# Kernel optimization log

Measured on AMD Instinct MI355X. Metric: run time of the kernel, lower is better.

## Reference

```python
import jax, jax.numpy as jnp
import numpy as np

K = 16          # neighbors (init kwarg k)
LEAK = 0.2      # LeakyReLU slope
EPS = 1e-5      # GroupNorm eps
GROUPS = 4


def knn_idx(coor_k, coor_q, k):
    # coor_* : (B, 3, N); returns (B, Nq, k) indices of k nearest keys per query
    qk = jnp.einsum('bdq,bdk->bqk', coor_q, coor_k)
    q2 = jnp.sum(coor_q * coor_q, axis=1)[:, :, None]
    k2 = jnp.sum(coor_k * coor_k, axis=1)[:, None, :]
    d2 = q2 + k2 - 2.0 * qk                     # (B, Nq, Nk) squared distances
    _, idx = jax.lax.top_k(-d2, k)
    return idx


def gather_feats(x_k, idx):
    # x_k (B, D, Nk), idx (B, Nq, k) -> (B, D, Nq, k)
    feat = jax.vmap(lambda fk, i: fk[i])(jnp.transpose(x_k, (0, 2, 1)), idx)  # (B,Nq,k,D)
    return jnp.transpose(feat, (0, 3, 1, 2))


def graph_feature(coor_q, x_q, coor_k, x_k, k):
    idx = knn_idx(coor_k, coor_q, k)
    feat = gather_feats(x_k, idx)                # (B, D, Nq, k)
    xq = x_q[:, :, :, None]
    return jnp.concatenate([feat - xq, jnp.broadcast_to(xq, feat.shape)], axis=1)


def group_norm(x, gamma, beta):
    B, C, N, Kk = x.shape
    xg = x.reshape(B, GROUPS, C // GROUPS, N, Kk)
    mu = xg.mean(axis=(2, 3, 4), keepdims=True)
    var = xg.var(axis=(2, 3, 4), keepdims=True)
    xn = ((xg - mu) * jax.lax.rsqrt(var + EPS)).reshape(B, C, N, Kk)
    return xn * gamma[None, :, None, None] + beta[None, :, None, None]


def conv_gn_lrelu(x, w, gamma, beta):
    y = jnp.einsum('oc,bcnk->bonk', w, x)        # 1x1 conv, no bias
    y = group_norm(y, gamma, beta)
    return jnp.where(y > 0, y, LEAK * y)


def fps(xyz, npoint):
    # xyz (B, N, 3) -> (B, npoint) farthest-point-sampling indices, start at 0
    B, N, _ = xyz.shape
    d0 = jnp.full((B, N), 1e10, dtype=xyz.dtype)

    def step(carry, _):
        dist, far = carry
        centroid = jnp.take_along_axis(xyz, far[:, None, None], axis=1)  # (B,1,3)
        d = jnp.sum((xyz - centroid) ** 2, axis=-1)
        dist = jnp.minimum(dist, d)
        nxt = jnp.argmax(dist, axis=-1).astype(jnp.int32)
        return (dist, nxt), far

    far0 = jnp.zeros((B,), dtype=jnp.int32)
    _, idxs = jax.lax.scan(step, (d0, far0), None, length=npoint)
    return jnp.transpose(idxs)                   # (B, npoint)


def fps_downsample(coor, x, num_group):
    # coor (B,3,N), x (B,D,N)
    fidx = fps(jnp.transpose(coor, (0, 2, 1)), num_group)   # (B, num_group)
    comb = jnp.concatenate([coor, x], axis=1)                # (B, 3+D, N)
    new = jax.vmap(lambda c, i: c[:, i])(comb, fidx)         # (B, 3+D, num_group)
    return new[:, :3], new[:, 3:]


def setup_inputs() -> dict:
    key = jax.random.key(0)
    ks = jax.random.split(key, 8)
    B, N = 16, 2048
    return {
        'x': jax.random.normal(ks[0], (B, N, 3), jnp.float32),
        'num0': 512,
        'num1': 128,
        'w_in': jax.random.normal(ks[1], (8, 3), jnp.float32) * 0.3,
        'b_in': jax.random.normal(ks[2], (8,), jnp.float32) * 0.1,
        'w1': jax.random.normal(ks[3], (32, 16), jnp.float32) * 0.2,
        'g1': jnp.ones((32,), jnp.float32), 'be1': jnp.zeros((32,), jnp.float32),
        'w2': jax.random.normal(ks[4], (64, 64), jnp.float32) * 0.12,
        'g2': jnp.ones((64,), jnp.float32), 'be2': jnp.zeros((64,), jnp.float32),
        'w3': jax.random.normal(ks[5], (64, 128), jnp.float32) * 0.09,
        'g3': jnp.ones((64,), jnp.float32), 'be3': jnp.zeros((64,), jnp.float32),
        'w4': jax.random.normal(ks[6], (128, 128), jnp.float32) * 0.09,
        'g4': jnp.ones((128,), jnp.float32), 'be4': jnp.zeros((128,), jnp.float32),
    }


def reference(x, num0, num1, w_in, b_in, w1, g1, be1, w2, g2, be2,
              w3, g3, be3, w4, g4, be4):
    coor = jnp.transpose(x, (0, 2, 1))                       # (B,3,N)
    f = jnp.einsum('oc,bcn->bon', w_in, coor) + b_in[None, :, None]  # (B,8,N)

    f = graph_feature(coor, f, coor, f, K)                   # (B,16,N,K)
    f = conv_gn_lrelu(f, w1, g1, be1).max(axis=-1)           # (B,32,N)

    coor_q, f_q = fps_downsample(coor, f, num0)
    f = graph_feature(coor_q, f_q, coor, f, K)               # (B,64,num0,K)
    f = conv_gn_lrelu(f, w2, g2, be2).max(axis=-1)           # (B,64,num0)
    coor = coor_q

    f = graph_feature(coor, f, coor, f, K)                   # (B,128,num0,K)
    f = conv_gn_lrelu(f, w3, g3, be3).max(axis=-1)           # (B,64,num0)

    coor_q, f_q = fps_downsample(coor, f, num1)
    f = graph_feature(coor_q, f_q, coor, f, K)               # (B,128,num1,K)
    f = conv_gn_lrelu(f, w4, g4, be4).max(axis=-1)           # (B,128,num1)

    return jnp.transpose(coor_q, (0, 2, 1)), jnp.transpose(f, (0, 2, 1))
```

## Files before the change

### kernel.cpp

```cpp
#include <hip/hip_runtime.h>

#define KNN 16
static constexpr int BB = 16;
static constexpr float LEAK = 0.2f;
static constexpr float EPSV = 1e-5f;
typedef unsigned long long u64;

__device__ __forceinline__ void ce_asc(u64 &a, u64 &b) {
  u64 x = a, y = b; bool sw = y < x; a = sw ? y : x; b = sw ? x : y;
}
__device__ __forceinline__ void ce_desc(u64 &a, u64 &b) {
  u64 x = a, y = b; bool sw = x < y; a = sw ? y : x; b = sw ? x : y;
}
__device__ __forceinline__ void bitonic_sort16(u64 *T) {
#pragma unroll
  for (int k = 2; k <= 16; k <<= 1) {
#pragma unroll
    for (int j = k >> 1; j > 0; j >>= 1) {
#pragma unroll
      for (int i = 0; i < 16; ++i) {
        int l = i ^ j;
        if (l > i) {
          if ((i & k) == 0) ce_asc(T[i], T[l]); else ce_desc(T[i], T[l]);
        }
      }
    }
  }
}
__device__ __forceinline__ void merge_sorted16(u64 *R, const u64 *T) {
#pragma unroll
  for (int i = 0; i < 16; ++i) {
    u64 t = T[15 - i];
    R[i] = t < R[i] ? t : R[i];
  }
#pragma unroll
  for (int j = 8; j > 0; j >>= 1) {
#pragma unroll
    for (int i = 0; i < 16; ++i) {
      int l = i ^ j;
      if (l > i) ce_asc(R[i], R[l]);
    }
  }
}
template<int KC>
__device__ __forceinline__ void merge_row(const u64* __restrict__ p, u64* R) {
#pragma unroll
  for (int s = 0; s < 16; ++s) R[s] = p[s];
#pragma unroll
  for (int c = 1; c < KC; ++c) {
    u64 T[16];
#pragma unroll
    for (int s = 0; s < 16; ++s) T[s] = p[(size_t)c*KNN + s];
    merge_sorted16(R, T);
  }
}

__device__ __forceinline__ void f0_dev(const float* __restrict__ x,
    const float* __restrict__ w_in, const float* __restrict__ b_in,
    float* __restrict__ f0, int bid) {
  int i = bid * 256 + threadIdx.x;
  float px = x[i*3+0], py = x[i*3+1], pz = x[i*3+2];
#pragma unroll
  for (int o = 0; o < 8; ++o) {
    f0[i*8+o] = w_in[o*3+0]*px + w_in[o*3+1]*py + w_in[o*3+2]*pz + b_in[o];
  }
}

__device__ void knn_part_dev(const float* __restrict__ qxyz, int Nq,
    const float* __restrict__ kxyz, int Nk, int KC, u64* __restrict__ part,
    char* sm, int bid) {
  float4* keys = (float4*)sm;
  int nqb = (Nq + 255) >> 8;
  int c  = bid % KC;
  int qb = (bid / KC) % nqb;
  int b  = bid / (KC * nqb);
  int nkc = Nk / KC;
  int kbase = c * nkc;
  for (int j = threadIdx.x; j < nkc; j += 256) {
    const float* kp = kxyz + (size_t)(b*Nk + kbase + j)*3;
    float kx = kp[0], ky = kp[1], kz = kp[2];
    keys[j] = make_float4(kx, ky, kz, kx*kx + ky*ky + kz*kz);
  }
  __syncthreads();
  int q = (qb << 8) + threadIdx.x;
  if (q >= Nq) return;
  const float* qp = qxyz + (size_t)(b*Nq + q)*3;
  float qx = qp[0], qy = qp[1], qz = qp[2];
  float q2 = qx*qx + qy*qy + qz*qz;
  u64 R[16];
#pragma unroll
  for (int s = 0; s < 16; ++s) R[s] = 0xFFFFFFFFFFFFFFFFull;
  for (int j0 = 0; j0 < nkc; j0 += 16) {
    u64 T[16];
#pragma unroll
    for (int u = 0; u < 16; ++u) {
      float4 kk = keys[j0 + u];
      float qk = qx*kk.x + qy*kk.y + qz*kk.z;
      float d2 = q2 + kk.w - 2.0f*qk;
      int bb = __float_as_int(d2);
      unsigned k32 = (unsigned)bb ^ (unsigned)((bb >> 31) | 0x80000000);
      T[u] = ((u64)k32 << 32) | (unsigned)(kbase + j0 + u);
    }
    bitonic_sort16(T);
    merge_sorted16(R, T);
  }
  u64* op = part + ((size_t)(b*Nq + q)*KC + c)*KNN;
#pragma unroll
  for (int s = 0; s < KNN; ++s) op[s] = R[s];
}

__device__ __forceinline__ u64 fps_max64(u64 a, u64 b) { return a > b ? a : b; }
template<int CTRL>
__device__ __forceinline__ float fps_dpp_fmax(float v) {
  int nb = __builtin_amdgcn_update_dpp(0, __float_as_int(v), CTRL, 0xF, 0xF, false);
  return fmaxf(v, __int_as_float(nb));
}
template<int P, bool SAVE>
__device__ void fps_seg_dev(const float* __restrict__ xyz, int np,
    int t0, int t1, int* __restrict__ fidx,
    float* __restrict__ g_dl, int* __restrict__ g_far,
    int* __restrict__ inv, float* __restrict__ cq, char* sm, int b) {
  constexpr int NN = P * 256;
  float4* sc  = (float4*)sm;
  int* s_fid  = (int*)(sm + NN*16);
  u64* s_key  = (u64*)(sm + NN*16 + 2048);
  __builtin_amdgcn_s_setprio(1);
  int tid = threadIdx.x;
  int w = tid >> 6, lw = tid & 63;
  float px[P], py[P], pz[P], dl[P];
#pragma unroll
  for (int i = 0; i < P; ++i) {
    int p = tid * P + i;
    const float* pp = xyz + (size_t)(b*NN + p)*3;
    px[i] = pp[0]; py[i] = pp[1]; pz[i] = pp[2];
    sc[p] = make_float4(px[i], py[i], pz[i], 0.f);
  }
  int far;
  if (t0 == 0) {
#pragma unroll
    for (int i = 0; i < P; ++i) dl[i] = 1e10f;
    far = 0;
  } else {
#pragma unroll
    for (int i = 0; i < P; ++i) dl[i] = g_dl[b*NN + tid*P + i];
    far = g_far[b];
  }
  __syncthreads();
  for (int t = t0; t < t1; ++t) {
    if (tid == 0) { fidx[b*np + t] = far; s_fid[t] = far; }
    float4 cc = sc[far];
#pragma unroll
    for (int i = 0; i < P; ++i) {
      float dx = __fsub_rn(px[i], cc.x);
      float dy = __fsub_rn(py[i], cc.y);
      float dz = __fsub_rn(pz[i], cc.z);
      float d = __fadd_rn(__fadd_rn(__fmul_rn(dx,dx), __fmul_rn(dy,dy)), __fmul_rn(dz,dz));
      dl[i] = fminf(dl[i], d);
    }
    float m[P];
#pragma unroll
    for (int i = 0; i < P; ++i) m[i] = dl[i];
#pragma unroll
    for (int st = P/2; st > 0; st >>= 1) {
#pragma unroll
      for (int i = 0; i < P; ++i) if (i < st) m[i] = fmaxf(m[i], m[i + st]);
    }
    float lmax = m[0];
    unsigned msk = 0u;
#pragma unroll
    for (int i = 0; i < P; ++i) msk |= (dl[i] == lmax) ? (1u << i) : 0u;
    int lidx = tid * P + __builtin_ctz(msk);
    float v = lmax;
    v = fps_dpp_fmax<0x111>(v);
    v = fps_dpp_fmax<0x112>(v);
    v = fps_dpp_fmax<0x114>(v);
    v = fps_dpp_fmax<0x118>(v);
    v = fps_dpp_fmax<0x142>(v);
    v = fps_dpp_fmax<0x143>(v);
    float wmax = __int_as_float(__builtin_amdgcn_readlane(__float_as_int(v), 63));
    u64 bal = __ballot(lmax == wmax);
    int l0 = __ffsll((unsigned long long)bal) - 1;
    int wp = __builtin_amdgcn_readlane(lidx, l0);
    int buf = t & 1;
    if (lw == 0)
      s_key[buf*4 + w] = ((u64)__float_as_uint(wmax) << 32) | (unsigned)(~wp);
    __syncthreads();
    u64 best = s_key[buf*4 + 0];
    best = fps_max64(best, s_key[buf*4 + 1]);
    best = fps_max64(best, s_key[buf*4 + 2]);
    best = fps_max64(best, s_key[buf*4 + 3]);
    far = (int)(~(unsigned)(best & 0xFFFFFFFFull));
  }
  if constexpr (SAVE) {
#pragma unroll
    for (int i = 0; i < P; ++i) g_dl[b*NN + tid*P + i] = dl[i];
    if (tid == 0) g_far[b] = far;
  } else {
    __syncthreads();
    for (int j = tid; j < np; j += 256) {
      int p = (j >= t0) ? s_fid[j] : fidx[b*np + j];
      if (inv) inv[b*NN + p] = j;
      float4 c = sc[p];
      float* cp = cq + (size_t)(b*np + j)*3;
      cp[0] = c.x; cp[1] = c.y; cp[2] = c.z;
    }
  }
  __builtin_amdgcn_s_setprio(0);
}

__device__ __forceinline__ void fq1gather_dev(const float* __restrict__ f1,
    const int* __restrict__ fidx1, float* __restrict__ fq1, int bid) {
  int i = bid * 256 + threadIdx.x;
  int b = i >> 9;
  int src = fidx1[i];
  const float4* s = (const float4*)(f1 + (size_t)(b*2048 + src)*32);
  float4* d = (float4*)(fq1 + (size_t)i*32);
#pragma unroll
  for (int c = 0; c < 8; ++c) d[c] = s[c];
}

template<int C, int O, int QB, int KC, int NB>
__device__ void conv_dev(const float* __restrict__ fsrc, int Nsrc,
    const float* __restrict__ fq, int Nq, const u64* __restrict__ part,
    const float* __restrict__ w, float* __restrict__ ym, float* __restrict__ yn,
    double2* __restrict__ pp1, char* sm, int bid) {
  constexpr int Og = O / 4;
  constexpr int C4 = C / 4;
  double* rs  = (double*)sm;
  double* rs2 = rs + 256;
  float* ft   = (float*)(sm + 4096);
  float* fqs  = ft + QB*KNN*C;
  int* s_idx  = (int*)(fqs + QB*C);
  int tid = threadIdx.x;
  int chunk = bid % NB;
  int b = bid / NB;
  int q0 = chunk * QB;
  if (tid < QB) {
    const u64* p = part + (size_t)(b*Nq + q0 + tid)*KC*KNN;
    u64 R[16];
    merge_row<KC>(p, R);
#pragma unroll
    for (int s = 0; s < 16; ++s) s_idx[tid*KNN + s] = (int)(unsigned)(R[s] & 0xFFFFFFFFu);
  } else if (tid >= 64 && tid < 64 + QB*C4) {
    int t = tid - 64;
    int ql = t / C4, c4 = t % C4;
    ((float4*)&fqs[ql*C])[c4] = ((const float4*)(fq + (size_t)(b*Nq + q0 + ql)*C))[c4];
  }
  __syncthreads();
  for (int v = tid; v < QB*KNN*C4; v += 256) {
    int row = v / C4, c4 = v % C4;
    int ql = row / KNN, k = row % KNN;
    int src = s_idx[ql*KNN + k];
    ((float4*)&ft[(ql*KNN + k)*C])[c4] = ((const float4*)(fsrc + (size_t)(b*Nsrc + src)*C))[c4];
  }
  __syncthreads();
  int ql = tid / O, o = tid % O;
  float4 wr4[C4];
  float bs = 0.f;
  const float4* wp4 = (const float4*)(w + (size_t)o*2*C);
#pragma unroll
  for (int c4 = 0; c4 < C4; ++c4) {
    float4 lo = wp4[c4], hi = wp4[C4 + c4];
    float4 fv = ((const float4*)&fqs[ql*C])[c4];
    bs += (hi.x - lo.x) * fv.x;
    bs += (hi.y - lo.y) * fv.y;
    bs += (hi.z - lo.z) * fv.z;
    bs += (hi.w - lo.w) * fv.w;
    wr4[c4] = lo;
  }
  float mx = -3.4e38f, mn = 3.4e38f;
  double s = 0.0, s2 = 0.0;
  for (int k = 0; k < KNN; ++k) {
    float acc = bs;
    const float4* fv = (const float4*)&ft[(ql*KNN + k)*C];
#pragma unroll
    for (int c4 = 0; c4 < C4; ++c4) {
      float4 v = fv[c4];
      acc += wr4[c4].x*v.x; acc += wr4[c4].y*v.y;
      acc += wr4[c4].z*v.z; acc += wr4[c4].w*v.w;
    }
    mx = fmaxf(mx, acc);
    mn = fminf(mn, acc);
    s += acc;
    s2 += (double)acc * (double)acc;
  }
  size_t oidx = (size_t)(b*Nq + q0 + ql)*O + o;
  ym[oidx] = mx;
  yn[oidx] = mn;
  rs[tid] = s; rs2[tid] = s2;
  __syncthreads();
#pragma unroll
  for (int st = QB/2; st > 0; st >>= 1) {
    if (ql < st) { rs[tid] += rs[tid + st*O]; rs2[tid] += rs2[tid + st*O]; }
    __syncthreads();
  }
#pragma unroll
  for (int st = Og/2; st > 0; st >>= 1) {
    if (tid < O && (o % Og) < st) { rs[tid] += rs[tid + st]; rs2[tid] += rs2[tid + st]; }
    __syncthreads();
  }
  if (tid < O && (o % Og) == 0) {
    int g = o / Og;
    pp1[((size_t)b*NB + chunk)*4 + g] = make_double2(rs[tid], rs2[tid]);
  }
}

template<int O, int NB, int FCH, int NQ, int NSEL>
__device__ void fin_dev(const float* __restrict__ ym, const float* __restrict__ yn,
    const double2* __restrict__ pp1, const float* __restrict__ gamma,
    const float* __restrict__ beta, float* __restrict__ fout,
    const int* __restrict__ inv, float* __restrict__ fqout, char* sm, int bid) {
  constexpr int Og = O / 4;
  double* red  = (double*)sm;
  double* red2 = red + 64;
  float* s_mu  = (float*)(red2 + 64);
  float* s_rsv = s_mu + 4;
  int tid = threadIdx.x;
  int b = bid / FCH;
  int f = bid % FCH;
  if (tid < 64) {
    int g = tid >> 4, j = tid & 15;
    double s = 0.0, s2 = 0.0;
    for (int c = j; c < NB; c += 16) {
      double2 v = pp1[((size_t)b*NB + c)*4 + g];
      s += v.x; s2 += v.y;
    }
    red[tid] = s; red2[tid] = s2;
  }
  __syncthreads();
#pragma unroll
  for (int st = 8; st > 0; st >>= 1) {
    if (tid < 64 && (tid & 15) < st) { red[tid] += red[tid+st]; red2[tid] += red2[tid+st]; }
    __syncthreads();
  }
  if (tid < 4) {
    double cnt = (double)Og * (double)NQ * (double)KNN;
    double mu = red[tid*16] / cnt;
    double var = red2[tid*16] / cnt - mu*mu;
    s_mu[tid] = (float)mu;
    s_rsv[tid] = 1.0f / sqrtf((float)var + EPSV);
  }
  __syncthreads();
  constexpr int PER = NQ * O / FCH;
  int e0 = f * PER;
  for (int e = e0 + tid; e < e0 + PER; e += 256) {
    int q = e / O, o = e % O;
    int g = o / Og;
    size_t idx = (size_t)(b*NQ + q)*O + o;
    float ga = gamma[o], be = beta[o];
    float ysel = (ga >= 0.f) ? ym[idx] : yn[idx];
    float xn = (ysel - s_mu[g]) * s_rsv[g];
    float yv = xn*ga + be;
    yv = yv > 0.f ? yv : LEAK*yv;
    fout[idx] = yv;
    if constexpr (NSEL > 0) {
      int j = inv[b*NQ + q];
      if (j >= 0) fqout[(size_t)(b*NSEL + j)*O + o] = yv;
    }
  }
}

__global__ __launch_bounds__(256) void fusedA_kernel(const float* __restrict__ x,
    const float* __restrict__ w_in, const float* __restrict__ b_in,
    float* __restrict__ f0, u64* __restrict__ part, int* __restrict__ fidx1,
    float* __restrict__ g_dl, int* __restrict__ g_far) {
  extern __shared__ char sm[];
  int bid = blockIdx.x;
  if (bid < 16)        fps_seg_dev<8,true>(x, 512, 0, 280, fidx1, g_dl, g_far, nullptr, nullptr, sm, bid);
  else if (bid < 1040) knn_part_dev(x, 2048, x, 2048, 8, part, sm, bid - 16);
  else                 f0_dev(x, w_in, b_in, f0, bid - 1040);
}

__global__ __launch_bounds__(256) void conv1_kernel(const float* __restrict__ x,
    int* __restrict__ fidx1, float* __restrict__ g_dl, int* __restrict__ g_far,
    const float* __restrict__ f0, const u64* __restrict__ part,
    const float* __restrict__ w1, float* __restrict__ ym, float* __restrict__ yn,
    double2* __restrict__ pp1) {
  extern __shared__ char sm[];
  int bid = blockIdx.x;
  if (bid < 16) fps_seg_dev<8,true>(x, 512, 280, 460, fidx1, g_dl, g_far, nullptr, nullptr, sm, bid);
  else          conv_dev<8,32,8,8,256>(f0, 2048, f0, 2048, part, w1, ym, yn, pp1, sm, bid - 16);
}

__global__ __launch_bounds__(256) void fin1_kernel(const float* __restrict__ x,
    int* __restrict__ fidx1, float* __restrict__ g_dl, int* __restrict__ g_far,
    float* __restrict__ cq1,
    const float* __restrict__ ym, const float* __restrict__ yn,
    const double2* __restrict__ pp1, const float* __restrict__ g1,
    const float* __restrict__ be1, float* __restrict__ f1) {
  extern __shared__ char sm[];
  int bid = blockIdx.x;
  if (bid < 16) fps_seg_dev<8,false>(x, 512, 460, 512, fidx1, g_dl, g_far, nullptr, cq1, sm, bid);
  else          fin_dev<32,256,32,2048,0>(ym, yn, pp1, g1, be1, f1, nullptr, nullptr, sm, bid - 16);
}

__global__ __launch_bounds__(256) void fusedB_kernel(const float* __restrict__ cq1,
    const float* __restrict__ x, u64* __restrict__ part2, u64* __restrict__ part3,
    int* __restrict__ fidx2, float* __restrict__ g_dl, int* __restrict__ g_far,
    int* __restrict__ inv2, const float* __restrict__ f1, const int* __restrict__ fidx1,
    float* __restrict__ fq1) {
  extern __shared__ char sm[];
  int bid = blockIdx.x;
  if (bid < 16) {
    fps_seg_dev<2,true>(cq1, 128, 0, 100, fidx2, g_dl, g_far, nullptr, nullptr, sm, bid);
  } else if (bid < 272) {
    if (bid < 48) inv2[(bid - 16)*256 + threadIdx.x] = -1;
    knn_part_dev(cq1, 512, x, 2048, 8, part2, sm, bid - 16);
  } else if (bid < 528) {
    knn_part_dev(cq1, 512, cq1, 512, 8, part3, sm, bid - 272);
  } else {
    fq1gather_dev(f1, fidx1, fq1, bid - 528);
  }
}

__global__ __launch_bounds__(256) void conv2_kernel(const float* __restrict__ cq1,
    int* __restrict__ fidx2, float* __restrict__ g_dl, int* __restrict__ g_far,
    int* __restrict__ inv2, float* __restrict__ cq2,
    const float* __restrict__ f1, const float* __restrict__ fq1,
    const u64* __restrict__ part2, const float* __restrict__ w2,
    float* __restrict__ ym, float* __restrict__ yn, double2* __restrict__ pp1) {
  extern __shared__ char sm[];
  int bid = blockIdx.x;
  if (bid < 16) fps_seg_dev<2,false>(cq1, 128, 100, 128, fidx2, g_dl, g_far, inv2, cq2, sm, bid);
  else          conv_dev<32,64,4,8,128>(f1, 2048, fq1, 512, part2, w2, ym, yn, pp1, sm, bid - 16);
}

__global__ __launch_bounds__(256) void fin2_kernel(const float* __restrict__ ym,
    const float* __restrict__ yn, const double2* __restrict__ pp1,
    const float* __restrict__ g2, const float* __restrict__ be2,
    float* __restrict__ f2) {
  extern __shared__ char sm[];
  fin_dev<64,128,16,512,0>(ym, yn, pp1, g2, be2, f2, nullptr, nullptr, sm, blockIdx.x);
}

__global__ __launch_bounds__(256) void conv3k4_kernel(const float* __restrict__ cq2,
    const float* __restrict__ cq1, u64* __restrict__ part4,
    const float* __restrict__ f2, const u64* __restrict__ part3,
    const float* __restrict__ w3, float* __restrict__ ym, float* __restrict__ yn,
    double2* __restrict__ pp1) {
  extern __shared__ char sm[];
  int bid = blockIdx.x;
  if (bid < 128) knn_part_dev(cq2, 128, cq1, 512, 8, part4, sm, bid);
  else           conv_dev<64,64,4,8,128>(f2, 512, f2, 512, part3, w3, ym, yn, pp1, sm, bid - 128);
}

__global__ __launch_bounds__(256) void fin3_kernel(const float* __restrict__ ym,
    const float* __restrict__ yn, const double2* __restrict__ pp1,
    const float* __restrict__ g3, const float* __restrict__ be3,
    float* __restrict__ f3, const int* __restrict__ inv2, float* __restrict__ fq2) {
  extern __shared__ char sm[];
  fin_dev<64,128,16,512,128>(ym, yn, pp1, g3, be3, f3, inv2, fq2, sm, blockIdx.x);
}

__global__ __launch_bounds__(256) void conv4_kernel(const float* __restrict__ f3,
    const float* __restrict__ fq2, const u64* __restrict__ part4,
    const float* __restrict__ w4, float* __restrict__ ym, float* __restrict__ yn,
    double2* __restrict__ pp1) {
  extern __shared__ char sm[];
  conv_dev<64,128,2,8,64>(f3, 512, fq2, 128, part4, w4, ym, yn, pp1, sm, blockIdx.x);
}

__global__ __launch_bounds__(256) void fin4_kernel(const float* __restrict__ ym,
    const float* __restrict__ yn, const double2* __restrict__ pp1,
    const float* __restrict__ g4, const float* __restrict__ be4,
    float* __restrict__ f4) {
  extern __shared__ char sm[];
  fin_dev<128,64,8,128,0>(ym, yn, pp1, g4, be4, f4, nullptr, nullptr, sm, blockIdx.x);
}

extern "C" void kernel_launch(void* const* d_in, const int* in_sizes, int n_in,
                              void* d_out, int out_size, void* d_ws, size_t ws_size,
                              hipStream_t stream) {
  const float* x    = (const float*)d_in[0];
  const float* w_in = (const float*)d_in[3];
  const float* b_in = (const float*)d_in[4];
  const float* w1 = (const float*)d_in[5];
  const float* g1 = (const float*)d_in[6];
  const float* be1= (const float*)d_in[7];
  const float* w2 = (const float*)d_in[8];
  const float* g2 = (const float*)d_in[9];
  const float* be2= (const float*)d_in[10];
  const float* w3 = (const float*)d_in[11];
  const float* g3 = (const float*)d_in[12];
  const float* be3= (const float*)d_in[13];
  const float* w4 = (const float*)d_in[14];
  const float* g4 = (const float*)d_in[15];
  const float* be4= (const float*)d_in[16];
  float* out = (float*)d_out;
  (void)in_sizes; (void)n_in; (void)out_size; (void)ws_size;

  char* ws = (char*)d_ws;
  size_t off = 0;
  auto alloc = [&](size_t count) {
    void* p = ws + off;
    off += (count * 4 + 255) & ~(size_t)255;
    return p;
  };
  float* f0    = (float*)alloc(16*2048*8);
  float* f1    = (float*)alloc(16*2048*32);
  float* f2    = (float*)alloc(16*512*64);
  float* f3    = (float*)alloc(16*512*64);
  float* fq1   = (float*)alloc(16*512*32);
  float* fq2   = (float*)alloc(16*128*64);
  float* cq1   = (float*)alloc(16*512*3);
  float* ym    = (float*)alloc(16*2048*32);
  float* yn    = (float*)alloc(16*2048*32);
  double2* pp1 = (double2*)alloc(16*256*4*4);
  int* fidx1   = (int*)alloc(16*512);
  int* fidx2   = (int*)alloc(16*128);
  int* inv2    = (int*)alloc(16*512);
  float* g_dl1 = (float*)alloc(16*2048);
  int* g_far1  = (int*)alloc(16);
  float* g_dl2 = (float*)alloc(16*512);
  int* g_far2  = (int*)alloc(16);
  u64* part1 = (u64*)alloc((size_t)2 * 16*2048*8*16);
  u64* part2 = part1;
  u64* part3 = part1 + (size_t)16*512*8*16;
  u64* part4 = part1 + (size_t)2*16*512*8*16;

  float* cq2 = out;
  float* f4  = out + 16*128*3;

  constexpr size_t SM_F1  = 2048*16 + 2048 + 64;
  constexpr size_t SM_F2  = 512*16 + 2048 + 64;
  constexpr size_t SM_KNN = 4096;
  constexpr size_t SM_C1  = 4096 + 8*KNN*8*4 + 8*8*4 + 8*KNN*4;
  constexpr size_t SM_C2  = 4096 + 4*KNN*32*4 + 4*32*4 + 4*KNN*4;
  constexpr size_t SM_C3  = 4096 + 4*KNN*64*4 + 4*64*4 + 4*KNN*4;
  constexpr size_t SM_C4  = 4096 + 2*KNN*64*4 + 2*64*4 + 2*KNN*4;
  constexpr size_t SM_FIN = 1056;
  auto mx2 = [](size_t a, size_t b) { return a > b ? a : b; };

  fusedA_kernel<<<1168, 256, mx2(SM_F1, SM_KNN), stream>>>(x, w_in, b_in, f0, part1, fidx1, g_dl1, g_far1);
  conv1_kernel<<<4112, 256, mx2(SM_F1, SM_C1), stream>>>(x, fidx1, g_dl1, g_far1, f0, part1, w1, ym, yn, pp1);
  fin1_kernel<<<528, 256, mx2(SM_F1, SM_FIN), stream>>>(x, fidx1, g_dl1, g_far1, cq1, ym, yn, pp1, g1, be1, f1);

  fusedB_kernel<<<560, 256, mx2(SM_F2, SM_KNN), stream>>>(cq1, x, part2, part3, fidx2, g_dl2, g_far2, inv2, f1, fidx1, fq1);
  conv2_kernel<<<2064, 256, mx2(SM_F2, SM_C2), stream>>>(cq1, fidx2, g_dl2, g_far2, inv2, cq2, f1, fq1, part2, w2, ym, yn, pp1);
  fin2_kernel<<<256, 256, SM_FIN, stream>>>(ym, yn, pp1, g2, be2, f2);

  conv3k4_kernel<<<2176, 256, mx2(SM_KNN, SM_C3), stream>>>(cq2, cq1, part4, f2, part3, w3, ym, yn, pp1);
  fin3_kernel<<<256, 256, SM_FIN, stream>>>(ym, yn, pp1, g3, be3, f3, inv2, fq2);

  conv4_kernel<<<1024, 256, SM_C4, stream>>>(f3, fq2, part4, w4, ym, yn, pp1);
  fin4_kernel<<<128, 256, SM_FIN, stream>>>(ym, yn, pp1, g4, be4, f4);
}
```

Measured before the change: 470.5 us.

## Fold GroupNorm finalize into next conv gather and carry FPS centroid in registers

Removes the separate fin1/fin2/fin3 kernels. Each following conv kernel now reduces the previous layer's partial group statistics itself and applies the normalize plus LeakyReLU transform on the fly while gathering neighbor features from the raw max/min buffers. FPS no longer stages all coordinates in shared memory: the winning point's coordinates travel with the argmax key through readlane and LDS, which shrinks shared memory per block. The FPS split point moves from 280/460 to 300, and the fq gather and inverse-map work is dropped. In exchange, every conv block redundantly re-reduces the statistics and reads two buffers (max and min) per gathered element.

```diff
diff --git a/kernel.cpp b/kernel.cpp
--- a/kernel.cpp
+++ b/kernel.cpp
@@ -115,15 +115,18 @@
   int nb = __builtin_amdgcn_update_dpp(0, __float_as_int(v), CTRL, 0xF, 0xF, false);
   return fmaxf(v, __int_as_float(nb));
 }
+__device__ __forceinline__ float rl_f(float v, int l) {
+  return __int_as_float(__builtin_amdgcn_readlane(__float_as_int(v), l));
+}
 template<int P, bool SAVE>
 __device__ void fps_seg_dev(const float* __restrict__ xyz, int np,
     int t0, int t1, int* __restrict__ fidx,
     float* __restrict__ g_dl, int* __restrict__ g_far,
-    int* __restrict__ inv, float* __restrict__ cq, char* sm, int b) {
+    float* __restrict__ cq, char* sm, int b) {
   constexpr int NN = P * 256;
-  float4* sc  = (float4*)sm;
-  int* s_fid  = (int*)(sm + NN*16);
-  u64* s_key  = (u64*)(sm + NN*16 + 2048);
+  int* s_fid   = (int*)sm;
+  u64* s_key   = (u64*)(sm + 2048);
+  float4* s_cc = (float4*)(sm + 2112);
   __builtin_amdgcn_s_setprio(1);
   int tid = threadIdx.x;
   int w = tid >> 6, lw = tid & 63;
@@ -133,7 +136,6 @@
     int p = tid * P + i;
     const float* pp = xyz + (size_t)(b*NN + p)*3;
     px[i] = pp[0]; py[i] = pp[1]; pz[i] = pp[2];
-    sc[p] = make_float4(px[i], py[i], pz[i], 0.f);
   }
   int far;
   if (t0 == 0) {
@@ -145,15 +147,15 @@
     for (int i = 0; i < P; ++i) dl[i] = g_dl[b*NN + tid*P + i];
     far = g_far[b];
   }
-  __syncthreads();
+  const float* fp = xyz + (size_t)(b*NN + far)*3;
+  float ccx = fp[0], ccy = fp[1], ccz = fp[2];
   for (int t = t0; t < t1; ++t) {
     if (tid == 0) { fidx[b*np + t] = far; s_fid[t] = far; }
-    float4 cc = sc[far];
 #pragma unroll
     for (int i = 0; i < P; ++i) {
-      float dx = __fsub_rn(px[i], cc.x);
-      float dy = __fsub_rn(py[i], cc.y);
-      float dz = __fsub_rn(pz[i], cc.z);
+      float dx = __fsub_rn(px[i], ccx);
+      float dy = __fsub_rn(py[i], ccy);
+      float dz = __fsub_rn(pz[i], ccz);
       float d = __fadd_rn(__fadd_rn(__fmul_rn(dx,dx), __fmul_rn(dy,dy)), __fmul_rn(dz,dz));
       dl[i] = fminf(dl[i], d);
     }
@@ -170,6 +172,14 @@
 #pragma unroll
     for (int i = 0; i < P; ++i) msk |= (dl[i] == lmax) ? (1u << i) : 0u;
     int lidx = tid * P + __builtin_ctz(msk);
+    float cxl = px[P-1], cyl = py[P-1], czl = pz[P-1];
+#pragma unroll
+    for (int i = P-1; i >= 0; --i) {
+      bool tk = (msk >> i) & 1u;
+      cxl = tk ? px[i] : cxl;
+      cyl = tk ? py[i] : cyl;
+      czl = tk ? pz[i] : czl;
+    }
     float v = lmax;
     v = fps_dpp_fmax<0x111>(v);
     v = fps_dpp_fmax<0x112>(v);
@@ -177,19 +187,24 @@
     v = fps_dpp_fmax<0x118>(v);
     v = fps_dpp_fmax<0x142>(v);
     v = fps_dpp_fmax<0x143>(v);
-    float wmax = __int_as_float(__builtin_amdgcn_readlane(__float_as_int(v), 63));
+    float wmax = rl_f(v, 63);
     u64 bal = __ballot(lmax == wmax);
     int l0 = __ffsll((unsigned long long)bal) - 1;
     int wp = __builtin_amdgcn_readlane(lidx, l0);
+    float wcx = rl_f(cxl, l0), wcy = rl_f(cyl, l0), wcz = rl_f(czl, l0);
     int buf = t & 1;
-    if (lw == 0)
+    if (lw == 0) {
       s_key[buf*4 + w] = ((u64)__float_as_uint(wmax) << 32) | (unsigned)(~wp);
+      s_cc[buf*4 + w] = make_float4(wcx, wcy, wcz, 0.f);
+    }
     __syncthreads();
-    u64 best = s_key[buf*4 + 0];
-    best = fps_max64(best, s_key[buf*4 + 1]);
-    best = fps_max64(best, s_key[buf*4 + 2]);
-    best = fps_max64(best, s_key[buf*4 + 3]);
-    far = (int)(~(unsigned)(best & 0xFFFFFFFFull));
+    u64 k0 = s_key[buf*4+0], k1 = s_key[buf*4+1], k2 = s_key[buf*4+2], k3 = s_key[buf*4+3];
+    float4 c0 = s_cc[buf*4+0], c1 = s_cc[buf*4+1], c2 = s_cc[buf*4+2], c3 = s_cc[buf*4+3];
+    if (k1 > k0) { k0 = k1; c0 = c1; }
+    if (k3 > k2) { k2 = k3; c2 = c3; }
+    if (k2 > k0) { k0 = k2; c0 = c2; }
+    far = (int)(~(unsigned)(k0 & 0xFFFFFFFFull));
+    ccx = c0.x; ccy = c0.y; ccz = c0.z;
   }
   if constexpr (SAVE) {
 #pragma unroll
@@ -199,38 +214,44 @@
     __syncthreads();
     for (int j = tid; j < np; j += 256) {
       int p = (j >= t0) ? s_fid[j] : fidx[b*np + j];
-      if (inv) inv[b*NN + p] = j;
-      float4 c = sc[p];
+      const float* sp = xyz + (size_t)(b*NN + p)*3;
       float* cp = cq + (size_t)(b*np + j)*3;
-      cp[0] = c.x; cp[1] = c.y; cp[2] = c.z;
+      cp[0] = sp[0]; cp[1] = sp[1]; cp[2] = sp[2];
     }
   }
   __builtin_amdgcn_s_setprio(0);
 }
 
-__device__ __forceinline__ void fq1gather_dev(const float* __restrict__ f1,
-    const int* __restrict__ fidx1, float* __restrict__ fq1, int bid) {
-  int i = bid * 256 + threadIdx.x;
-  int b = i >> 9;
-  int src = fidx1[i];
-  const float4* s = (const float4*)(f1 + (size_t)(b*2048 + src)*32);
-  float4* d = (float4*)(fq1 + (size_t)i*32);
-#pragma unroll
-  for (int c = 0; c < 8; ++c) d[c] = s[c];
-}
-
-template<int C, int O, int QB, int KC, int NB>
-__device__ void conv_dev(const float* __restrict__ fsrc, int Nsrc,
-    const float* __restrict__ fq, int Nq, const u64* __restrict__ part,
-    const float* __restrict__ w, float* __restrict__ ym, float* __restrict__ yn,
-    double2* __restrict__ pp1, char* sm, int bid) {
+__device__ __forceinline__ float xform1(float m, float n, float ga, float be,
+                                        float mu, float rsv) {
+  float ysel = (ga >= 0.f) ? m : n;
+  float xn = (ysel - mu) * rsv;
+  float yv = xn*ga + be;
+  return yv > 0.f ? yv : LEAK*yv;
+}
+
+template<int C, int O, int QB, int KC, int NB, bool XF, int NBP, int NQP>
+__device__ void conv_dev(const float* __restrict__ fsrc,
+    const float* __restrict__ ymP, const float* __restrict__ ynP, int Nsrc,
+    const int* __restrict__ qmap, int Nq, const u64* __restrict__ part,
+    const float* __restrict__ w, const double2* __restrict__ ppP,
+    const float* __restrict__ gaP, const float* __restrict__ beP,
+    float* __restrict__ ym, float* __restrict__ yn, double2* __restrict__ pp1,
+    char* sm, int bid) {
   constexpr int Og = O / 4;
   constexpr int C4 = C / 4;
-  double* rs  = (double*)sm;
-  double* rs2 = rs + 256;
-  float* ft   = (float*)(sm + 4096);
-  float* fqs  = ft + QB*KNN*C;
-  int* s_idx  = (int*)(fqs + QB*C);
+  double* rs    = (double*)sm;
+  double* rs2   = rs + 256;
+  double* sred  = rs2 + 256;
+  double* sred2 = sred + 64;
+  float* s_mu   = (float*)(sred2 + 64);
+  float* s_rsv  = s_mu + 4;
+  float* s_ga   = s_rsv + 4;
+  float* s_be   = s_ga + 64;
+  int*   s_idx  = (int*)(s_be + 64);
+  float* fqs    = (float*)(s_idx + QB*16);
+  float* fqn    = fqs + QB*C;
+  float* ft     = fqn + QB*C;
   int tid = threadIdx.x;
   int chunk = bid % NB;
   int b = bid / NB;
@@ -241,17 +262,79 @@
     merge_row<KC>(p, R);
 #pragma unroll
     for (int s = 0; s < 16; ++s) s_idx[tid*KNN + s] = (int)(unsigned)(R[s] & 0xFFFFFFFFu);
-  } else if (tid >= 64 && tid < 64 + QB*C4) {
-    int t = tid - 64;
-    int ql = t / C4, c4 = t % C4;
-    ((float4*)&fqs[ql*C])[c4] = ((const float4*)(fq + (size_t)(b*Nq + q0 + ql)*C))[c4];
+  } else if (XF && tid >= 64 && tid < 128) {
+    int tt = tid - 64, g = tt >> 4, j = tt & 15;
+    double s = 0.0, s2 = 0.0;
+    for (int c = j; c < NBP; c += 16) {
+      double2 v = ppP[((size_t)b*NBP + c)*4 + g];
+      s += v.x; s2 += v.y;
+    }
+    sred[tt] = s; sred2[tt] = s2;
+  } else if (XF && tid >= 128 && tid < 128 + C) {
+    int c = tid - 128;
+    s_ga[c] = gaP[c]; s_be[c] = beP[c];
+  } else if (tid >= 192 && tid < 192 + QB*C4) {
+    int tt = tid - 192;
+    int ql = tt / C4, c4 = tt % C4;
+    int q = q0 + ql;
+    int sq = qmap ? qmap[b*Nq + q] : q;
+    if constexpr (XF) {
+      ((float4*)fqs)[ql*C4 + c4] = ((const float4*)(ymP + (size_t)(b*Nsrc + sq)*C))[c4];
+      ((float4*)fqn)[ql*C4 + c4] = ((const float4*)(ynP + (size_t)(b*Nsrc + sq)*C))[c4];
+    } else {
+      ((float4*)fqs)[ql*C4 + c4] = ((const float4*)(fsrc + (size_t)(b*Nsrc + sq)*C))[c4];
+    }
   }
   __syncthreads();
+  if constexpr (XF) {
+    if (tid < 4) {
+      double a[16], a2[16];
+#pragma unroll
+      for (int j = 0; j < 16; ++j) { a[j] = sred[tid*16 + j]; a2[j] = sred2[tid*16 + j]; }
+#pragma unroll
+      for (int st = 8; st > 0; st >>= 1) {
+#pragma unroll
+        for (int j = 0; j < 8; ++j) if (j < st) { a[j] += a[j+st]; a2[j] += a2[j+st]; }
+      }
+      double cnt = (double)C4 * (double)NQP * (double)KNN;
+      double mu = a[0] / cnt;
+      double var = a2[0] / cnt - mu*mu;
+      s_mu[tid] = (float)mu;
+      s_rsv[tid] = 1.0f / sqrtf((float)var + EPSV);
+    }
+    __syncthreads();
+  }
   for (int v = tid; v < QB*KNN*C4; v += 256) {
     int row = v / C4, c4 = v % C4;
     int ql = row / KNN, k = row % KNN;
     int src = s_idx[ql*KNN + k];
-    ((float4*)&ft[(ql*KNN + k)*C])[c4] = ((const float4*)(fsrc + (size_t)(b*Nsrc + src)*C))[c4];
+    if constexpr (XF) {
+      float4 mv = ((const float4*)(ymP + (size_t)(b*Nsrc + src)*C))[c4];
+      float4 nv = ((const float4*)(ynP + (size_t)(b*Nsrc + src)*C))[c4];
+      int cb = c4*4;
+      float4 r;
+      r.x = xform1(mv.x, nv.x, s_ga[cb+0], s_be[cb+0], s_mu[(cb+0)/C4], s_rsv[(cb+0)/C4]);
+      r.y = xform1(mv.y, nv.y, s_ga[cb+1], s_be[cb+1], s_mu[(cb+1)/C4], s_rsv[(cb+1)/C4]);
+      r.z = xform1(mv.z, nv.z, s_ga[cb+2], s_be[cb+2], s_mu[(cb+2)/C4], s_rsv[(cb+2)/C4]);
+      r.w = xform1(mv.w, nv.w, s_ga[cb+3], s_be[cb+3], s_mu[(cb+3)/C4], s_rsv[(cb+3)/C4]);
+      ((float4*)ft)[row*C4 + c4] = r;
+    } else {
+      ((float4*)ft)[row*C4 + c4] = ((const float4*)(fsrc + (size_t)(b*Nsrc + src)*C))[c4];
+    }
+  }
+  if constexpr (XF) {
+    if (tid < QB*C4) {
+      int ql = tid / C4, c4 = tid % C4;
+      float4 mv = ((float4*)fqs)[ql*C4 + c4];
+      float4 nv = ((float4*)fqn)[ql*C4 + c4];
+      int cb = c4*4;
+      float4 r;
+      r.x = xform1(mv.x, nv.x, s_ga[cb+0], s_be[cb+0], s_mu[(cb+0)/C4], s_rsv[(cb+0)/C4]);
+      r.y = xform1(mv.y, nv.y, s_ga[cb+1], s_be[cb+1], s_mu[(cb+1)/C4], s_rsv[(cb+1)/C4]);
+      r.z = xform1(mv.z, nv.z, s_ga[cb+2], s_be[cb+2], s_mu[(cb+2)/C4], s_rsv[(cb+2)/C4]);
+      r.w = xform1(mv.w, nv.w, s_ga[cb+3], s_be[cb+3], s_mu[(cb+3)/C4], s_rsv[(cb+3)/C4]);
+      ((float4*)fqs)[ql*C4 + c4] = r;
+    }
   }
   __syncthreads();
   int ql = tid / O, o = tid % O;
@@ -275,9 +358,9 @@
     const float4* fv = (const float4*)&ft[(ql*KNN + k)*C];
 #pragma unroll
     for (int c4 = 0; c4 < C4; ++c4) {
-      float4 v = fv[c4];
-      acc += wr4[c4].x*v.x; acc += wr4[c4].y*v.y;
-      acc += wr4[c4].z*v.z; acc += wr4[c4].w*v.w;
+      float4 vv = fv[c4];
+      acc += wr4[c4].x*vv.x; acc += wr4[c4].y*vv.y;
+      acc += wr4[c4].z*vv.z; acc += wr4[c4].w*vv.w;
     }
     mx = fmaxf(mx, acc);
     mn = fminf(mn, acc);
@@ -305,11 +388,10 @@
   }
 }
 
-template<int O, int NB, int FCH, int NQ, int NSEL>
+template<int O, int NB, int FCH, int NQ>
 __device__ void fin_dev(const float* __restrict__ ym, const float* __restrict__ yn,
     const double2* __restrict__ pp1, const float* __restrict__ gamma,
-    const float* __restrict__ beta, float* __restrict__ fout,
-    const int* __restrict__ inv, float* __restrict__ fqout, char* sm, int bid) {
+    const float* __restrict__ beta, float* __restrict__ fout, char* sm, int bid) {
   constexpr int Og = O / 4;
   double* red  = (double*)sm;
   double* red2 = red + 64;
@@ -347,16 +429,7 @@
     int q = e / O, o = e % O;
     int g = o / Og;
     size_t idx = (size_t)(b*NQ + q)*O + o;
-    float ga = gamma[o], be = beta[o];
-    float ysel = (ga >= 0.f) ? ym[idx] : yn[idx];
-    float xn = (ysel - s_mu[g]) * s_rsv[g];
-    float yv = xn*ga + be;
-    yv = yv > 0.f ? yv : LEAK*yv;
-    fout[idx] = yv;
-    if constexpr (NSEL > 0) {
-      int j = inv[b*NQ + q];
-      if (j >= 0) fqout[(size_t)(b*NSEL + j)*O + o] = yv;
-    }
+    fout[idx] = xform1(ym[idx], yn[idx], gamma[o], beta[o], s_mu[g], s_rsv[g]);
   }
 }
 
@@ -366,106 +439,79 @@
     float* __restrict__ g_dl, int* __restrict__ g_far) {
   extern __shared__ char sm[];
   int bid = blockIdx.x;
-  if (bid < 16)        fps_seg_dev<8,true>(x, 512, 0, 280, fidx1, g_dl, g_far, nullptr, nullptr, sm, bid);
+  if (bid < 16)        fps_seg_dev<8,true>(x, 512, 0, 300, fidx1, g_dl, g_far, nullptr, sm, bid);
   else if (bid < 1040) knn_part_dev(x, 2048, x, 2048, 8, part, sm, bid - 16);
   else                 f0_dev(x, w_in, b_in, f0, bid - 1040);
 }
 
 __global__ __launch_bounds__(256) void conv1_kernel(const float* __restrict__ x,
     int* __restrict__ fidx1, float* __restrict__ g_dl, int* __restrict__ g_far,
-    const float* __restrict__ f0, const u64* __restrict__ part,
-    const float* __restrict__ w1, float* __restrict__ ym, float* __restrict__ yn,
-    double2* __restrict__ pp1) {
+    float* __restrict__ cq1, const float* __restrict__ f0,
+    const u64* __restrict__ part, const float* __restrict__ w1,
+    float* __restrict__ ymA, float* __restrict__ ynA, double2* __restrict__ ppA) {
   extern __shared__ char sm[];
   int bid = blockIdx.x;
-  if (bid < 16) fps_seg_dev<8,true>(x, 512, 280, 460, fidx1, g_dl, g_far, nullptr, nullptr, sm, bid);
-  else          conv_dev<8,32,8,8,256>(f0, 2048, f0, 2048, part, w1, ym, yn, pp1, sm, bid - 16);
-}
-
-__global__ __launch_bounds__(256) void fin1_kernel(const float* __restrict__ x,
-    int* __restrict__ fidx1, float* __restrict__ g_dl, int* __restrict__ g_far,
-    float* __restrict__ cq1,
-    const float* __restrict__ ym, const float* __restrict__ yn,
-    const double2* __restrict__ pp1, const float* __restrict__ g1,
-    const float* __restrict__ be1, float* __restrict__ f1) {
-  extern __shared__ char sm[];
-  int bid = blockIdx.x;
-  if (bid < 16) fps_seg_dev<8,false>(x, 512, 460, 512, fidx1, g_dl, g_far, nullptr, cq1, sm, bid);
-  else          fin_dev<32,256,32,2048,0>(ym, yn, pp1, g1, be1, f1, nullptr, nullptr, sm, bid - 16);
+  if (bid < 16) fps_seg_dev<8,false>(x, 512, 300, 512, fidx1, g_dl, g_far, cq1, sm, bid);
+  else conv_dev<8,32,8,8,256,false,1,1>(f0, nullptr, nullptr, 2048, nullptr, 2048,
+                part, w1, nullptr, nullptr, nullptr, ymA, ynA, ppA, sm, bid - 16);
 }
 
 __global__ __launch_bounds__(256) void fusedB_kernel(const float* __restrict__ cq1,
     const float* __restrict__ x, u64* __restrict__ part2, u64* __restrict__ part3,
-    int* __restrict__ fidx2, float* __restrict__ g_dl, int* __restrict__ g_far,
-    int* __restrict__ inv2, const float* __restrict__ f1, const int* __restrict__ fidx1,
-    float* __restrict__ fq1) {
+    int* __restrict__ fidx2, float* __restrict__ g_dl, int* __restrict__ g_far) {
   extern __shared__ char sm[];
   int bid = blockIdx.x;
-  if (bid < 16) {
-    fps_seg_dev<2,true>(cq1, 128, 0, 100, fidx2, g_dl, g_far, nullptr, nullptr, sm, bid);
-  } else if (bid < 272) {
-    if (bid < 48) inv2[(bid - 16)*256 + threadIdx.x] = -1;
-    knn_part_dev(cq1, 512, x, 2048, 8, part2, sm, bid - 16);
-  } else if (bid < 528) {
-    knn_part_dev(cq1, 512, cq1, 512, 8, part3, sm, bid - 272);
-  } else {
-    fq1gather_dev(f1, fidx1, fq1, bid - 528);
-  }
+  if (bid < 16)       fps_seg_dev<2,true>(cq1, 128, 0, 100, fidx2, g_dl, g_far, nullptr, sm, bid);
+  else if (bid < 272) knn_part_dev(cq1, 512, x, 2048, 8, part2, sm, bid - 16);
+  else                knn_part_dev(cq1, 512, cq1, 512, 8, part3, sm, bid - 272);
 }
 
 __global__ __launch_bounds__(256) void conv2_kernel(const float* __restrict__ cq1,
     int* __restrict__ fidx2, float* __restrict__ g_dl, int* __restrict__ g_far,
-    int* __restrict__ inv2, float* __restrict__ cq2,
-    const float* __restrict__ f1, const float* __restrict__ fq1,
-    const u64* __restrict__ part2, const float* __restrict__ w2,
-    float* __restrict__ ym, float* __restrict__ yn, double2* __restrict__ pp1) {
+    float* __restrict__ cq2,
+    const float* __restrict__ ymA, const float* __restrict__ ynA,
+    const int* __restrict__ fidx1, const u64* __restrict__ part2,
+    const float* __restrict__ w2, const double2* __restrict__ ppA,
+    const float* __restrict__ g1, const float* __restrict__ be1,
+    float* __restrict__ ymB, float* __restrict__ ynB, double2* __restrict__ ppB) {
   extern __shared__ char sm[];
   int bid = blockIdx.x;
-  if (bid < 16) fps_seg_dev<2,false>(cq1, 128, 100, 128, fidx2, g_dl, g_far, inv2, cq2, sm, bid);
-  else          conv_dev<32,64,4,8,128>(f1, 2048, fq1, 512, part2, w2, ym, yn, pp1, sm, bid - 16);
-}
-
-__global__ __launch_bounds__(256) void fin2_kernel(const float* __restrict__ ym,
-    const float* __restrict__ yn, const double2* __restrict__ pp1,
-    const float* __restrict__ g2, const float* __restrict__ be2,
-    float* __restrict__ f2) {
-  extern __shared__ char sm[];
-  fin_dev<64,128,16,512,0>(ym, yn, pp1, g2, be2, f2, nullptr, nullptr, sm, blockIdx.x);
+  if (bid < 16) fps_seg_dev<2,false>(cq1, 128, 100, 128, fidx2, g_dl, g_far, cq2, sm, bid);
+  else conv_dev<32,64,4,8,128,true,256,2048>(nullptr, ymA, ynA, 2048, fidx1, 512,
+                part2, w2, ppA, g1, be1, ymB, ynB, ppB, sm, bid - 16);
 }
 
 __global__ __launch_bounds__(256) void conv3k4_kernel(const float* __restrict__ cq2,
     const float* __restrict__ cq1, u64* __restrict__ part4,
-    const float* __restrict__ f2, const u64* __restrict__ part3,
-    const float* __restrict__ w3, float* __restrict__ ym, float* __restrict__ yn,
-    double2* __restrict__ pp1) {
+    const float* __restrict__ ymB, const float* __restrict__ ynB,
+    const u64* __restrict__ part3, const float* __restrict__ w3,
+    const double2* __restrict__ ppB, const float* __restrict__ g2,
+    const float* __restrict__ be2,
+    float* __restrict__ ymA, float* __restrict__ ynA, double2* __restrict__ ppA) {
   extern __shared__ char sm[];
   int bid = blockIdx.x;
   if (bid < 128) knn_part_dev(cq2, 128, cq1, 512, 8, part4, sm, bid);
-  else           conv_dev<64,64,4,8,128>(f2, 512, f2, 512, part3, w3, ym, yn, pp1, sm, bid - 128);
-}
-
-__global__ __launch_bounds__(256) void fin3_kernel(const float* __restrict__ ym,
-    const float* __restrict__ yn, const double2* __restrict__ pp1,
+  else conv_dev<64,64,4,8,128,true,128,512>(nullptr, ymB, ynB, 512, nullptr, 512,
+                part3, w3, ppB, g2, be2, ymA, ynA, ppA, sm, bid - 128);
+}
+
+__global__ __launch_bounds__(256) void conv4_kernel(
+    const float* __restrict__ ymA, const float* __restrict__ ynA,
+    const int* __restrict__ fidx2, const u64* __restrict__ part4,
+    const float* __restrict__ w4, const double2* __restrict__ ppA,
     const float* __restrict__ g3, const float* __restrict__ be3,
-    float* __restrict__ f3, const int* __restrict__ inv2, float* __restrict__ fq2) {
-  extern __shared__ char sm[];
-  fin_dev<64,128,16,512,128>(ym, yn, pp1, g3, be3, f3, inv2, fq2, sm, blockIdx.x);
-}
-
-__global__ __launch_bounds__(256) void conv4_kernel(const float* __restrict__ f3,
-    const float* __restrict__ fq2, const u64* __restrict__ part4,
-    const float* __restrict__ w4, float* __restrict__ ym, float* __restrict__ yn,
-    double2* __restrict__ pp1) {
-  extern __shared__ char sm[];
-  conv_dev<64,128,2,8,64>(f3, 512, fq2, 128, part4, w4, ym, yn, pp1, sm, blockIdx.x);
-}
-
-__global__ __launch_bounds__(256) void fin4_kernel(const float* __restrict__ ym,
-    const float* __restrict__ yn, const double2* __restrict__ pp1,
+    float* __restrict__ ymB, float* __restrict__ ynB, double2* __restrict__ ppB) {
+  extern __shared__ char sm[];
+  conv_dev<64,128,2,8,64,true,128,512>(nullptr, ymA, ynA, 512, fidx2, 128,
+                part4, w4, ppA, g3, be3, ymB, ynB, ppB, sm, blockIdx.x);
+}
+
+__global__ __launch_bounds__(256) void fin4_kernel(const float* __restrict__ ymB,
+    const float* __restrict__ ynB, const double2* __restrict__ ppB,
     const float* __restrict__ g4, const float* __restrict__ be4,
     float* __restrict__ f4) {
   extern __shared__ char sm[];
-  fin_dev<128,64,8,128,0>(ym, yn, pp1, g4, be4, f4, nullptr, nullptr, sm, blockIdx.x);
+  fin_dev<128,64,8,128>(ymB, ynB, ppB, g4, be4, f4, sm, blockIdx.x);
 }
 
 extern "C" void kernel_launch(void* const* d_in, const int* in_sizes, int n_in,
@@ -497,18 +543,15 @@
     return p;
   };
   float* f0    = (float*)alloc(16*2048*8);
-  float* f1    = (float*)alloc(16*2048*32);
-  float* f2    = (float*)alloc(16*512*64);
-  float* f3    = (float*)alloc(16*512*64);
-  float* fq1   = (float*)alloc(16*512*32);
-  float* fq2   = (float*)alloc(16*128*64);
+  float* ymA   = (float*)alloc(16*2048*32);
+  float* ynA   = (float*)alloc(16*2048*32);
+  float* ymB   = (float*)alloc(16*512*64);
+  float* ynB   = (float*)alloc(16*512*64);
   float* cq1   = (float*)alloc(16*512*3);
-  float* ym    = (float*)alloc(16*2048*32);
-  float* yn    = (float*)alloc(16*2048*32);
-  double2* pp1 = (double2*)alloc(16*256*4*4);
+  double2* ppA = (double2*)alloc(16*256*4*4);
+  double2* ppB = (double2*)alloc(16*256*4*4);
   int* fidx1   = (int*)alloc(16*512);
   int* fidx2   = (int*)alloc(16*128);
-  int* inv2    = (int*)alloc(16*512);
   float* g_dl1 = (float*)alloc(16*2048);
   int* g_far1  = (int*)alloc(16);
   float* g_dl2 = (float*)alloc(16*512);
@@ -521,27 +564,22 @@
   float* cq2 = out;
   float* f4  = out + 16*128*3;
 
-  constexpr size_t SM_F1  = 2048*16 + 2048 + 64;
-  constexpr size_t SM_F2  = 512*16 + 2048 + 64;
+  constexpr size_t SM_FPS = 2240;
   constexpr size_t SM_KNN = 4096;
-  constexpr size_t SM_C1  = 4096 + 8*KNN*8*4 + 8*8*4 + 8*KNN*4;
-  constexpr size_t SM_C2  = 4096 + 4*KNN*32*4 + 4*32*4 + 4*KNN*4;
-  constexpr size_t SM_C3  = 4096 + 4*KNN*64*4 + 4*64*4 + 4*KNN*4;
-  constexpr size_t SM_C4  = 4096 + 2*KNN*64*4 + 2*64*4 + 2*KNN*4;
+  constexpr size_t SM_C1  = 5664 + 8*16*4 + 2*8*8*4  + 8*16*8*4;
+  constexpr size_t SM_C2  = 5664 + 4*16*4 + 2*4*32*4 + 4*16*32*4;
+  constexpr size_t SM_C3  = 5664 + 4*16*4 + 2*4*64*4 + 4*16*64*4;
+  constexpr size_t SM_C4  = 5664 + 2*16*4 + 2*2*64*4 + 2*16*64*4;
   constexpr size_t SM_FIN = 1056;
   auto mx2 = [](size_t a, size_t b) { return a > b ? a : b; };
 
-  fusedA_kernel<<<1168, 256, mx2(SM_F1, SM_KNN), stream>>>(x, w_in, b_in, f0, part1, fidx1, g_dl1, g_far1);
-  conv1_kernel<<<4112, 256, mx2(SM_F1, SM_C1), stream>>>(x, fidx1, g_dl1, g_far1, f0, part1, w1, ym, yn, pp1);
-  fin1_kernel<<<528, 256, mx2(SM_F1, SM_FIN), stream>>>(x, fidx1, g_dl1, g_far1, cq1, ym, yn, pp1, g1, be1, f1);
-
-  fusedB_kernel<<<560, 256, mx2(SM_F2, SM_KNN), stream>>>(cq1, x, part2, part3, fidx2, g_dl2, g_far2, inv2, f1, fidx1, fq1);
-  conv2_kernel<<<2064, 256, mx2(SM_F2, SM_C2), stream>>>(cq1, fidx2, g_dl2, g_far2, inv2, cq2, f1, fq1, part2, w2, ym, yn, pp1);
-  fin2_kernel<<<256, 256, SM_FIN, stream>>>(ym, yn, pp1, g2, be2, f2);
-
-  conv3k4_kernel<<<2176, 256, mx2(SM_KNN, SM_C3), stream>>>(cq2, cq1, part4, f2, part3, w3, ym, yn, pp1);
-  fin3_kernel<<<256, 256, SM_FIN, stream>>>(ym, yn, pp1, g3, be3, f3, inv2, fq2);
-
-  conv4_kernel<<<1024, 256, SM_C4, stream>>>(f3, fq2, part4, w4, ym, yn, pp1);
-  fin4_kernel<<<128, 256, SM_FIN, stream>>>(ym, yn, pp1, g4, be4, f4);
-}
+  fusedA_kernel<<<1168, 256, mx2(SM_FPS, SM_KNN), stream>>>(x, w_in, b_in, f0, part1, fidx1, g_dl1, g_far1);
+  conv1_kernel<<<4112, 256, mx2(SM_FPS, SM_C1), stream>>>(x, fidx1, g_dl1, g_far1, cq1, f0, part1, w1, ymA, ynA, ppA);
+  fusedB_kernel<<<528, 256, mx2(SM_FPS, SM_KNN), stream>>>(cq1, x, part2, part3, fidx2, g_dl2, g_far2);
+  conv2_kernel<<<2064, 256, mx2(SM_FPS, SM_C2), stream>>>(cq1, fidx2, g_dl2, g_far2, cq2,
+      ymA, ynA, fidx1, part2, w2, ppA, g1, be1, ymB, ynB, ppB);
+  conv3k4_kernel<<<2176, 256, mx2(SM_KNN, SM_C3), stream>>>(cq2, cq1, part4,
+      ymB, ynB, part3, w3, ppB, g2, be2, ymA, ynA, ppA);
+  conv4_kernel<<<1024, 256, SM_C4, stream>>>(ymA, ynA, fidx2, part4, w4, ppA, g3, be3, ymB, ynB, ppB);
+  fin4_kernel<<<128, 256, SM_FIN, stream>>>(ymB, ynB, ppB, g4, be4, f4);
+}
```

After: 498.9 us. +6.0%, slower.
